# Optimization experiments

Measured on AMD Instinct MI355X. Metric: run time of the kernel, lower is better.

Reference implementation:

```python
import jax, jax.numpy as jnp
import numpy as np

B, S, D, DIM = 8, 4096, 1024, 512  # batch, src nodes, dst nodes, feature dim


def setup_inputs() -> dict:
    key = jax.random.key(0)
    k1, k2, k3, k4, k5 = jax.random.split(key, 5)
    scale = 1.0 / np.sqrt(DIM)
    return {
        "src_val": jax.random.normal(k1, (B, S, DIM), dtype=jnp.float32),
        "src_state": jax.random.normal(k2, (B, S), dtype=jnp.float32),
        "dst_val": jax.random.normal(k3, (B, D, DIM), dtype=jnp.float32),
        "W_route": jax.random.normal(k4, (DIM, DIM), dtype=jnp.float32) * scale,
        "W_val": jax.random.normal(k5, (DIM, DIM), dtype=jnp.float32) * scale,
    }


def reference(src_val, src_state, dst_val, W_route, W_val):
    # Pairwise route logits: bilinear bipartite attention, [B, S, D]
    inv_sqrt_d = 1.0 / jnp.sqrt(jnp.asarray(src_val.shape[-1], src_val.dtype))
    q = jnp.einsum("bsd,de->bse", src_val, W_route)
    logits = jnp.einsum("bse,bke->bsk", q, dst_val) * inv_sqrt_d
    # route compression: softmax over dst nodes (dim=-1)
    routes = jax.nn.softmax(logits, axis=-1)
    # projections
    projected_val = jnp.einsum("bsd,de->bse", src_val, W_val)  # [B, S, DIM]
    projected_state = src_state                                 # identity state proj, [B, S]
    sender_strength = jax.nn.softplus(src_state)                # [B, S]
    # weighted routing + accumulation
    weighted_routes = routes * sender_strength[..., None]       # [B, S, D]
    delta_state = jnp.einsum("bsk,bs->bk", weighted_routes, projected_state)   # [B, D]
    delta_val = jnp.einsum("bsk,bsd->bkd", weighted_routes, projected_val)     # [B, D, DIM]
    return delta_state, delta_val
```

## Files before the change

### kernel.cpp

```cpp
#include <hip/hip_runtime.h>
#include <hip/hip_fp16.h>

#define B_   8
#define S_   4096
#define DD_  1024
#define DIM_ 512
#define SCALE 0.044194173824159216f

typedef __bf16 bf16x8 __attribute__((ext_vector_type(8)));
typedef float  floatx4 __attribute__((ext_vector_type(4)));

__device__ inline unsigned short f2bf(float f) {
    union { float f; unsigned int u; } v; v.f = f;
    unsigned int r = v.u + 0x7fffu + ((v.u >> 16) & 1u);
    return (unsigned short)(r >> 16);
}
__device__ inline float bf2f(unsigned short h) {
    union { unsigned int u; float f; } v; v.u = ((unsigned int)h) << 16;
    return v.f;
}
__device__ inline uint4 cvt8(const float* __restrict__ g) {
    float4 f0 = *(const float4*)g;
    float4 f1 = *(const float4*)(g + 4);
    unsigned short tmp[8] = {f2bf(f0.x), f2bf(f0.y), f2bf(f0.z), f2bf(f0.w),
                             f2bf(f1.x), f2bf(f1.y), f2bf(f1.z), f2bf(f1.w)};
    return *(const uint4*)tmp;
}
__device__ inline void async16(unsigned short* lds, const unsigned short* g) {
    __builtin_amdgcn_global_load_lds(
        (const __attribute__((address_space(1))) void*)g,
        (__attribute__((address_space(3))) void*)lds, 16, 0, 0);
}

__device__ inline void vwait8() { asm volatile("s_waitcnt vmcnt(8)" ::: "memory"); }
__device__ inline void vwait4() { asm volatile("s_waitcnt vmcnt(4)" ::: "memory"); }
__device__ inline void vwait0() { asm volatile("s_waitcnt vmcnt(0)" ::: "memory"); }
#define SBAR   __builtin_amdgcn_s_barrier()
#define SCHED0 __builtin_amdgcn_sched_barrier(0)

__device__ inline void mainloop256(unsigned short* As, unsigned short* Bs,
                                   const unsigned short* __restrict__ Ap, size_t lda,
                                   const unsigned short* __restrict__ Bp, size_t ldb,
                                   int nk, floatx4 (&acc)[8][4]) {
    const int t = threadIdx.x, lane = t & 63, w = t >> 6;
    const int wm = w >> 2, wn = w & 3;
    const int fr = lane & 15;
    const int swz  = (((lane >> 4) ^ ((fr >> 1) & 3)) << 3);
    const int csrc = (((t & 3) ^ ((t >> 3) & 3)) << 3);

    const unsigned short* gA = Ap + (size_t)(t >> 2) * lda + csrc;
    const unsigned short* gB = Bp + (size_t)(t >> 2) * ldb + csrc;
    unsigned short* ldsA = As + w * 512;
    unsigned short* ldsB = Bs + w * 512;

    auto stgA = [&](int buf, int kt, int kh) {
        const unsigned short* g = gA + (size_t)kt * 64 + kh * 32;
        async16(ldsA + buf * 16384 + kh * 8192,        g);
        async16(ldsA + buf * 16384 + kh * 8192 + 4096, g + (size_t)128 * lda);
    };
    auto stgB = [&](int buf, int kt, int kh) {
        const unsigned short* g = gB + (size_t)kt * 64 + kh * 32;
        async16(ldsB + buf * 16384 + kh * 8192,        g);
        async16(ldsB + buf * 16384 + kh * 8192 + 4096, g + (size_t)128 * ldb);
    };

    stgA(0, 0, 0); stgB(0, 0, 0); stgA(0, 0, 1); stgB(0, 0, 1);
    stgA(1, 1, 0); stgB(1, 1, 0);
    vwait8();
    SCHED0;
    SBAR;

    const int arow = wm * 128 + fr, brow = wn * 64 + fr;
    for (int kt = 0; kt < nk; ++kt) {
        const int cur = kt & 1;
        const bool sA = kt + 1 < nk, sB = kt + 2 < nk;
        const int base = cur * 16384;
        bf16x8 a[4], b[4], a2[4];
#pragma unroll
        for (int i = 0; i < 4; ++i)
            a[i] = *(const bf16x8*)&As[base + (arow + i * 16) * 32 + swz];
#pragma unroll
        for (int j = 0; j < 4; ++j)
            b[j] = *(const bf16x8*)&Bs[base + (brow + j * 16) * 32 + swz];
        if (sA) stgA(cur ^ 1, kt + 1, 1);
        SCHED0;
        SBAR;
        __builtin_amdgcn_s_setprio(1);
#pragma unroll
        for (int i = 0; i < 4; ++i)
#pragma unroll
            for (int j = 0; j < 4; ++j)
                acc[i][j] = __builtin_amdgcn_mfma_f32_16x16x32_bf16(a[i], b[j], acc[i][j], 0, 0, 0);
        __builtin_amdgcn_s_setprio(0);
        SBAR;
#pragma unroll
        for (int i = 0; i < 4; ++i)
            a2[i] = *(const bf16x8*)&As[base + (arow + 64 + i * 16) * 32 + swz];
        if (sA) stgB(cur ^ 1, kt + 1, 1);
        SCHED0;
        SBAR;
        __builtin_amdgcn_s_setprio(1);
#pragma unroll
        for (int i = 0; i < 4; ++i)
#pragma unroll
            for (int j = 0; j < 4; ++j)
                acc[4 + i][j] = __builtin_amdgcn_mfma_f32_16x16x32_bf16(a2[i], b[j], acc[4 + i][j], 0, 0, 0);
        __builtin_amdgcn_s_setprio(0);
        if (sA) vwait8(); else vwait0();
        SBAR;
#pragma unroll
        for (int i = 0; i < 4; ++i)
            a[i] = *(const bf16x8*)&As[base + 8192 + (arow + i * 16) * 32 + swz];
#pragma unroll
        for (int j = 0; j < 4; ++j)
            b[j] = *(const bf16x8*)&Bs[base + 8192 + (brow + j * 16) * 32 + swz];
        if (sB) stgA(cur, kt + 2, 0);
        SCHED0;
        SBAR;
        __builtin_amdgcn_s_setprio(1);
#pragma unroll
        for (int i = 0; i < 4; ++i)
#pragma unroll
            for (int j = 0; j < 4; ++j)
                acc[i][j] = __builtin_amdgcn_mfma_f32_16x16x32_bf16(a[i], b[j], acc[i][j], 0, 0, 0);
        __builtin_amdgcn_s_setprio(0);
        SBAR;
#pragma unroll
        for (int i = 0; i < 4; ++i)
            a2[i] = *(const bf16x8*)&As[base + 8192 + (arow + 64 + i * 16) * 32 + swz];
        if (sB) stgB(cur, kt + 2, 0);
        SCHED0;
        SBAR;
        __builtin_amdgcn_s_setprio(1);
#pragma unroll
        for (int i = 0; i < 4; ++i)
#pragma unroll
            for (int j = 0; j < 4; ++j)
                acc[4 + i][j] = __builtin_amdgcn_mfma_f32_16x16x32_bf16(a2[i], b[j], acc[4 + i][j], 0, 0, 0);
        __builtin_amdgcn_s_setprio(0);
        if (sA) { if (sB) vwait8(); else vwait4(); }
        SBAR;
    }
}

#define ACC_INIT8                                           \
    floatx4 acc[8][4];                                      \
    _Pragma("unroll") for (int i = 0; i < 8; ++i)           \
        _Pragma("unroll") for (int j = 0; j < 4; ++j)       \
            acc[i][j] = (floatx4){0.f, 0.f, 0.f, 0.f};

template <int AF32, int BF32>
__device__ inline void mainloop(unsigned short* As, unsigned short* Bs,
                                const void* Ap, size_t lda,
                                const void* Bp, size_t ldb,
                                int kIters, floatx4 (&acc)[4][4]) {
    const int t = threadIdx.x, lane = t & 63, wave = t >> 6;
    const int rA = t >> 2;
    const int cA = ((t & 3) ^ ((t >> 3) & 3)) * 8;
    const int mrow = (wave >> 1) * 64, ncol = (wave & 1) * 64;
    const int fr = lane & 15, fk = (lane >> 4) * 8;
    const int swz = (((fk >> 3) ^ ((fr >> 1) & 3)) << 3);

    const unsigned short* gA16 = nullptr; const float* gA32 = nullptr;
    const unsigned short* gB16 = nullptr; const float* gB32 = nullptr;
    if (AF32) gA32 = (const float*)Ap + (size_t)rA * lda + cA;
    else      gA16 = (const unsigned short*)Ap + (size_t)rA * lda + cA;
    if (BF32) gB32 = (const float*)Bp + (size_t)rA * ldb + cA;
    else      gB16 = (const unsigned short*)Bp + (size_t)rA * ldb + cA;

    unsigned short* ldsA = As + wave * 512;
    unsigned short* ldsB = Bs + wave * 512;

    auto stage = [&](int buf) {
        const int o = buf * 4096;
        if (AF32) {
            *(uint4*)&As[o + t * 8]        = cvt8(gA32);
            *(uint4*)&As[o + 2048 + t * 8] = cvt8(gA32 + 64 * lda);
            gA32 += 32;
        } else {
            async16(ldsA + o,        gA16);
            async16(ldsA + o + 2048, gA16 + 64 * lda);
            gA16 += 32;
        }
        if (BF32) {
            *(uint4*)&Bs[o + t * 8]        = cvt8(gB32);
            *(uint4*)&Bs[o + 2048 + t * 8] = cvt8(gB32 + 64 * ldb);
            gB32 += 32;
        } else {
            async16(ldsB + o,        gB16);
            async16(ldsB + o + 2048, gB16 + 64 * ldb);
            gB16 += 32;
        }
    };

    stage(0);
    __syncthreads();
    for (int kt = 0; kt < kIters; ++kt) {
        if (kt + 1 < kIters) stage((kt + 1) & 1);
        const int cur = (kt & 1) * 4096;
        bf16x8 af[4], bfr[4];
#pragma unroll
        for (int i = 0; i < 4; ++i)
            af[i] = *(const bf16x8*)&As[cur + (mrow + i * 16 + fr) * 32 + swz];
#pragma unroll
        for (int j = 0; j < 4; ++j)
            bfr[j] = *(const bf16x8*)&Bs[cur + (ncol + j * 16 + fr) * 32 + swz];
#pragma unroll
        for (int i = 0; i < 4; ++i)
#pragma unroll
            for (int j = 0; j < 4; ++j)
                acc[i][j] = __builtin_amdgcn_mfma_f32_16x16x32_bf16(af[i], bfr[j],
                                                                    acc[i][j], 0, 0, 0);
        __syncthreads();
    }
}

#define EPILOGUE_COORDS                                     \
    const int lane = threadIdx.x & 63, wave = threadIdx.x >> 6; \
    const int mrow = (wave >> 1) * 64, ncol = (wave & 1) * 64;  \
    const int col = lane & 15, q = lane >> 4;

#define ACC_INIT                                            \
    floatx4 acc[4][4];                                      \
    _Pragma("unroll") for (int i = 0; i < 4; ++i)           \
        _Pragma("unroll") for (int j = 0; j < 4; ++j)       \
            acc[i][j] = (floatx4){0.f, 0.f, 0.f, 0.f};

__global__ __launch_bounds__(256) void k_prep(const float* __restrict__ src,
                                              unsigned short* __restrict__ srcb) {
    const size_t idx = ((size_t)blockIdx.x * 256 + threadIdx.x) * 8;
    *(uint4*)&srcb[idx] = cvt8(src + idx);
}

__global__ __launch_bounds__(256) void k_dstWr(const float* __restrict__ dst,
                                               const float* __restrict__ Wr,
                                               unsigned short* __restrict__ DW) {
    __shared__ unsigned short As[2 * 128 * 32];
    __shared__ unsigned short Bs[2 * 128 * 32];
    const int n0 = blockIdx.x * 128, m0 = blockIdx.y * 128;
    ACC_INIT
    mainloop<1, 1>(As, Bs, dst + (size_t)m0 * DIM_, DIM_,
                   Wr + (size_t)n0 * DIM_, DIM_, DIM_ / 32, acc);
    EPILOGUE_COORDS
#pragma unroll
    for (int i = 0; i < 4; ++i)
#pragma unroll
        for (int j = 0; j < 4; ++j)
#pragma unroll
            for (int r = 0; r < 4; ++r)
                DW[(size_t)(m0 + mrow + i * 16 + q * 4 + r) * DIM_ +
                   n0 + ncol + j * 16 + col] = f2bf(acc[i][j][r] * SCALE);
}

__global__ __launch_bounds__(512) void k_logitsT(const unsigned short* __restrict__ DW,
                                                 const unsigned short* __restrict__ srcb,
                                                 unsigned short* __restrict__ LTb,
                                                 float* __restrict__ Lpart) {
    __shared__ __align__(16) unsigned short As[32768];
    __shared__ __align__(16) unsigned short Bs[32768];
    const int n = blockIdx.x;
    const int b = n & 7;
    const int rem = n >> 3;
    const int xs = rem >> 2;
    const int yd = rem & 3;
    const int n0 = xs * 256, m0 = yd * 256;
    ACC_INIT8
    mainloop256(As, Bs,
                DW + (size_t)b * DD_ * DIM_ + (size_t)m0 * DIM_, DIM_,
                srcb + (size_t)b * S_ * DIM_ + (size_t)n0 * DIM_, DIM_,
                DIM_ / 64, acc);
    const int t = threadIdx.x, lane = t & 63, w = t >> 6;
    const int wm = w >> 2, wn = w & 3;
    const int c16 = lane & 15, q = lane >> 4;
    const int row0 = m0 + wm * 128, col0 = n0 + wn * 64;
    unsigned short* LT = LTb + (size_t)b * DD_ * S_;
    float psum[4] = {0.f, 0.f, 0.f, 0.f};
#pragma unroll
    for (int i = 0; i < 8; ++i)
#pragma unroll
        for (int j = 0; j < 4; ++j)
#pragma unroll
            for (int r = 0; r < 4; ++r) {
                float e = __expf(acc[i][j][r]);
                LT[(size_t)(row0 + i * 16 + q * 4 + r) * S_ +
                   col0 + j * 16 + c16] = f2bf(e);
                psum[j] += e;
            }
    float* csum = (float*)As;
    const int slice = wm * 4 + q;
#pragma unroll
    for (int j = 0; j < 4; ++j)
        csum[slice * 256 + wn * 64 + j * 16 + c16] = psum[j];
    __syncthreads();
    if (t < 256) {
        float v = 0.f;
#pragma unroll
        for (int k = 0; k < 8; ++k) v += csum[k * 256 + t];
        Lpart[((size_t)b * 4 + yd) * S_ + n0 + t] = v;
    }
}

__global__ __launch_bounds__(256) void k_finalize(const float* __restrict__ state,
                                                  const float* __restrict__ Lpart,
                                                  float* __restrict__ scale) {
    const int i = blockIdx.x * 256 + threadIdx.x;
    const int b = i >> 12, s = i & (S_ - 1);
    float d = 0.f;
#pragma unroll
    for (int k = 0; k < 4; ++k) d += Lpart[((size_t)b * 4 + k) * S_ + s];
    const float st = state[i];
    const float sp = (st > 15.f) ? st : log1pf(__expf(st));
    scale[i] = sp / d;
}

__global__ __launch_bounds__(256) void k_srcT(const unsigned short* __restrict__ srcb,
                                              const float* __restrict__ scale,
                                              unsigned short* __restrict__ srcST) {
    __shared__ unsigned short Ts[64 * 65];
    const int s0 = blockIdx.x * 64, d0 = blockIdx.y * 64, b = blockIdx.z;
    const int t = threadIdx.x;
    {
        const int r = t >> 2, c0 = (t & 3) * 16;
        const unsigned short* g =
            srcb + (size_t)b * S_ * DIM_ + (size_t)(s0 + r) * DIM_ + d0 + c0;
        uint4 v0 = *(const uint4*)g;
        uint4 v1 = *(const uint4*)(g + 8);
        const unsigned short* e0 = (const unsigned short*)&v0;
        const unsigned short* e1 = (const unsigned short*)&v1;
        const float sc = scale[(size_t)b * S_ + s0 + r];
#pragma unroll
        for (int i = 0; i < 8; ++i) {
            Ts[r * 65 + c0 + i]     = f2bf(bf2f(e0[i]) * sc);
            Ts[r * 65 + c0 + 8 + i] = f2bf(bf2f(e1[i]) * sc);
        }
    }
    __syncthreads();
    {
        const int rr = t >> 2, c0 = (t & 3) * 16;
        unsigned short tmp[16];
#pragma unroll
        for (int j = 0; j < 16; ++j) tmp[j] = Ts[(c0 + j) * 65 + rr];
        unsigned short* o =
            srcST + (size_t)b * DIM_ * S_ + (size_t)(d0 + rr) * S_ + s0 + c0;
        *(uint4*)o = *(const uint4*)tmp;
        *(uint4*)(o + 8) = *(const uint4*)(tmp + 8);
    }
}

__global__ __launch_bounds__(256) void k_dstate(const unsigned short* __restrict__ LT,
                                                const float* __restrict__ state,
                                                const float* __restrict__ scale,
                                                float* __restrict__ out) {
    const int b = blockIdx.y;
    const int dd = blockIdx.x * 4 + (threadIdx.x >> 6);
    const int lane = threadIdx.x & 63;
    const unsigned short* row = LT + (size_t)b * DD_ * S_ + (size_t)dd * S_;
    const float* st = state + (size_t)b * S_;
    const float* sc = scale + (size_t)b * S_;

    float acc = 0.f;
#pragma unroll
    for (int it = 0; it < S_ / 512; ++it) {
        const int s = it * 512 + lane * 8;
        uint4 v = *(const uint4*)(row + s);
        const unsigned short* e = (const unsigned short*)&v;
        float4 f0 = *(const float4*)(st + s);
        float4 f1 = *(const float4*)(st + s + 4);
        float4 c0 = *(const float4*)(sc + s);
        float4 c1 = *(const float4*)(sc + s + 4);
        acc += bf2f(e[0]) * f0.x * c0.x + bf2f(e[1]) * f0.y * c0.y +
               bf2f(e[2]) * f0.z * c0.z + bf2f(e[3]) * f0.w * c0.w +
               bf2f(e[4]) * f1.x * c1.x + bf2f(e[5]) * f1.y * c1.y +
               bf2f(e[6]) * f1.z * c1.z + bf2f(e[7]) * f1.w * c1.w;
    }
#pragma unroll
    for (int off = 32; off; off >>= 1) acc += __shfl_down(acc, off);
    if (lane == 0) out[(size_t)b * DD_ + dd] = acc;
}

__global__ __launch_bounds__(512) void k_dU(const unsigned short* __restrict__ LTb,
                                            const unsigned short* __restrict__ srcST,
                                            __half* __restrict__ Pp) {
    __shared__ __align__(16) unsigned short As[32768];
    __shared__ __align__(16) unsigned short Bs[32768];
    const int n = blockIdx.x;
    const int qn = n >> 3;
    const int tile = qn & 7, zhi = qn >> 3;
    const int z = (n & 7) + 8 * zhi;
    const int b = z >> 2, ks = z & 3;
    const int xe = tile >> 2;
    const int yd = tile & 3;
    const int n0 = xe * 256, m0 = yd * 256;
    ACC_INIT8
    mainloop256(As, Bs,
                LTb + (size_t)b * DD_ * S_ + (size_t)m0 * S_ + ks * 1024, S_,
                srcST + (size_t)b * DIM_ * S_ + (size_t)n0 * S_ + ks * 1024, S_,
                1024 / 64, acc);
    const int t = threadIdx.x, lane = t & 63, w = t >> 6;
    const int wm = w >> 2, wn = w & 3;
    const int c16 = lane & 15, q = lane >> 4;
    const int row0 = m0 + wm * 128, col0 = n0 + wn * 64;
    __half* O = Pp + (size_t)ks * B_ * DD_ * DIM_ + (size_t)b * DD_ * DIM_;
#pragma unroll
    for (int i = 0; i < 8; ++i)
#pragma unroll
        for (int j = 0; j < 4; ++j)
#pragma unroll
            for (int r = 0; r < 4; ++r)
                O[(size_t)(row0 + i * 16 + q * 4 + r) * DIM_ +
                  col0 + j * 16 + c16] = __float2half(acc[i][j][r]);
}

__global__ __launch_bounds__(256) void k_reduceU(const __half* __restrict__ Pp,
                                                 unsigned short* __restrict__ U,
                                                 const float* __restrict__ Wv,
                                                 unsigned short* __restrict__ WvT) {
    __shared__ float Ts[64 * 68];
    const int t = threadIdx.x;
    if (blockIdx.x < 2048) {
        const size_t idx = ((size_t)blockIdx.x * 256 + t) * 8;
        const size_t n = (size_t)B_ * DD_ * DIM_;
        float o[8] = {0.f, 0.f, 0.f, 0.f, 0.f, 0.f, 0.f, 0.f};
#pragma unroll
        for (int ks = 0; ks < 4; ++ks) {
            uint4 v = *(const uint4*)(Pp + (size_t)ks * n + idx);
            const __half* h = (const __half*)&v;
#pragma unroll
            for (int j = 0; j < 8; ++j) o[j] += __half2float(h[j]);
        }
        unsigned short tmp[8];
#pragma unroll
        for (int j = 0; j < 8; ++j) tmp[j] = f2bf(o[j]);
        *(uint4*)&U[idx] = *(const uint4*)tmp;
        return;
    }
    const int n2 = blockIdx.x - 2048;
    const int d0 = (n2 & 7) * 64, e0 = (n2 >> 3) * 64;
    {
        const int r = t >> 2, c0 = (t & 3) * 16;
        const float* g = Wv + (size_t)(d0 + r) * DIM_ + e0 + c0;
#pragma unroll
        for (int i = 0; i < 4; ++i)
            *(float4*)&Ts[r * 68 + c0 + i * 4] = *(const float4*)(g + i * 4);
    }
    __syncthreads();
    {
        const int rr = t >> 2, c0 = (t & 3) * 16;
        unsigned short tmp[16];
#pragma unroll
        for (int j = 0; j < 16; ++j) tmp[j] = f2bf(Ts[(c0 + j) * 68 + rr]);
        unsigned short* o = WvT + (size_t)(e0 + rr) * DIM_ + d0 + c0;
        *(uint4*)o = *(const uint4*)tmp;
        *(uint4*)(o + 8) = *(const uint4*)(tmp + 8);
    }
}

__global__ __launch_bounds__(256) void k_dvalW(const unsigned short* __restrict__ U,
                                               const unsigned short* __restrict__ WvT,
                                               float* __restrict__ d_val) {
    __shared__ unsigned short As[2 * 128 * 32];
    __shared__ unsigned short Bs[2 * 128 * 32];
    const int n0 = blockIdx.x * 128, m0 = blockIdx.y * 128;
    ACC_INIT
    mainloop<0, 0>(As, Bs, U + (size_t)m0 * DIM_, DIM_,
                   WvT + (size_t)n0 * DIM_, DIM_, DIM_ / 32, acc);
    EPILOGUE_COORDS
#pragma unroll
    for (int i = 0; i < 4; ++i)
#pragma unroll
        for (int j = 0; j < 4; ++j)
#pragma unroll
            for (int r = 0; r < 4; ++r)
                d_val[(size_t)(m0 + mrow + i * 16 + q * 4 + r) * DIM_ +
                      n0 + ncol + j * 16 + col] = acc[i][j][r];
}

extern "C" void kernel_launch(void* const* d_in, const int* in_sizes, int n_in,
                              void* d_out, int out_size, void* d_ws, size_t ws_size,
                              hipStream_t stream) {
    const float* src   = (const float*)d_in[0];
    const float* state = (const float*)d_in[1];
    const float* dst   = (const float*)d_in[2];
    const float* Wr    = (const float*)d_in[3];
    const float* Wv    = (const float*)d_in[4];

    unsigned short* srcb = (unsigned short*)d_ws;
    __half* Pp = (__half*)d_ws;
    unsigned short* LT = srcb + (size_t)B_ * S_ * DIM_;
    unsigned short* U  = LT;
    unsigned short* WvT = U + (size_t)B_ * DD_ * DIM_;
    unsigned short* C = LT + (size_t)B_ * DD_ * S_;
    unsigned short* DW = C;
    float* Lpart = (float*)(DW + (size_t)B_ * DD_ * DIM_);
    unsigned short* srcST = C;

    float* d_state = (float*)d_out;
    float* d_val   = (float*)d_out + B_ * DD_;
    float* scale   = d_val;

    k_prep<<<dim3(8192), 256, 0, stream>>>(src, srcb);
    k_dstWr<<<dim3(DIM_ / 128, (B_ * DD_) / 128), 256, 0, stream>>>(dst, Wr, DW);
    k_logitsT<<<dim3(512), 512, 0, stream>>>(DW, srcb, LT, Lpart);
    k_finalize<<<dim3((B_ * S_) / 256), 256, 0, stream>>>(state, Lpart, scale);
    k_dstate<<<dim3(DD_ / 4, B_), 256, 0, stream>>>(LT, state, scale, d_state);
    k_srcT<<<dim3(S_ / 64, DIM_ / 64, B_), 256, 0, stream>>>(srcb, scale, srcST);
    k_dU<<<dim3(256), 512, 0, stream>>>(LT, srcST, Pp);
    k_reduceU<<<dim3(2048 + 64), 256, 0, stream>>>(Pp, U, Wv, WvT);
    k_dvalW<<<dim3(DIM_ / 128, (B_ * DD_) / 128), 256, 0, stream>>>(U, WvT, d_val);
}
```

Measured before the change: 278.9 us.

## Software-pipeline LDS fragment loads with MFMA in 256-tile GEMM mainloop

Restructures the 256x256 GEMM main loop so each quarter-step's LDS fragment reads are issued alongside the previous quarter's MFMAs, with fragments for the next k-tile prefetched at the end of each iteration. This cuts the barriers per iteration from eight to four and relaxes the vmcnt waits from 8 to 6. Launch bounds on the two big GEMM kernels now request 2 blocks per CU. Holding more fragment registers live together with the occupancy hint risks register spills or tighter scheduling constraints.

```diff
diff --git a/kernel.cpp b/kernel.cpp
--- a/kernel.cpp
+++ b/kernel.cpp
@@ -32,9 +32,12 @@
         (__attribute__((address_space(3))) void*)lds, 16, 0, 0);
 }
 
-__device__ inline void vwait8() { asm volatile("s_waitcnt vmcnt(8)" ::: "memory"); }
-__device__ inline void vwait4() { asm volatile("s_waitcnt vmcnt(4)" ::: "memory"); }
-__device__ inline void vwait0() { asm volatile("s_waitcnt vmcnt(0)" ::: "memory"); }
+template <int N> __device__ inline void vwait() {
+    if constexpr (N == 0)      asm volatile("s_waitcnt vmcnt(0)" ::: "memory");
+    else if constexpr (N == 4) asm volatile("s_waitcnt vmcnt(4)" ::: "memory");
+    else if constexpr (N == 6) asm volatile("s_waitcnt vmcnt(6)" ::: "memory");
+    else                       asm volatile("s_waitcnt vmcnt(8)" ::: "memory");
+}
 #define SBAR   __builtin_amdgcn_s_barrier()
 #define SCHED0 __builtin_amdgcn_sched_barrier(0)
 
@@ -66,79 +69,82 @@
 
     stgA(0, 0, 0); stgB(0, 0, 0); stgA(0, 0, 1); stgB(0, 0, 1);
     stgA(1, 1, 0); stgB(1, 1, 0);
-    vwait8();
+    vwait<8>();
     SCHED0;
     SBAR;
 
     const int arow = wm * 128 + fr, brow = wn * 64 + fr;
+    bf16x8 a0[4], b0[4], a1[4], a2[4], b2[4], a3[4];
+#pragma unroll
+    for (int i = 0; i < 4; ++i) a0[i] = *(const bf16x8*)&As[(arow + i * 16) * 32 + swz];
+#pragma unroll
+    for (int j = 0; j < 4; ++j) b0[j] = *(const bf16x8*)&Bs[(brow + j * 16) * 32 + swz];
+
     for (int kt = 0; kt < nk; ++kt) {
-        const int cur = kt & 1;
+        const int cur = kt & 1, base = cur * 16384;
         const bool sA = kt + 1 < nk, sB = kt + 2 < nk;
-        const int base = cur * 16384;
-        bf16x8 a[4], b[4], a2[4];
-#pragma unroll
-        for (int i = 0; i < 4; ++i)
-            a[i] = *(const bf16x8*)&As[base + (arow + i * 16) * 32 + swz];
-#pragma unroll
-        for (int j = 0; j < 4; ++j)
-            b[j] = *(const bf16x8*)&Bs[base + (brow + j * 16) * 32 + swz];
         if (sA) stgA(cur ^ 1, kt + 1, 1);
         SCHED0;
+        __builtin_amdgcn_s_setprio(1);
+#pragma unroll
+        for (int i = 0; i < 4; ++i)
+            a1[i] = *(const bf16x8*)&As[base + (arow + 64 + i * 16) * 32 + swz];
+#pragma unroll
+        for (int i = 0; i < 4; ++i)
+#pragma unroll
+            for (int j = 0; j < 4; ++j)
+                acc[i][j] = __builtin_amdgcn_mfma_f32_16x16x32_bf16(a0[i], b0[j], acc[i][j], 0, 0, 0);
+        __builtin_amdgcn_s_setprio(0);
+        if (sA) vwait<6>(); else vwait<0>();
         SBAR;
+        if (sA) stgB(cur ^ 1, kt + 1, 1);
+        SCHED0;
         __builtin_amdgcn_s_setprio(1);
 #pragma unroll
         for (int i = 0; i < 4; ++i)
+            a2[i] = *(const bf16x8*)&As[base + 8192 + (arow + i * 16) * 32 + swz];
+#pragma unroll
+        for (int j = 0; j < 4; ++j)
+            b2[j] = *(const bf16x8*)&Bs[base + 8192 + (brow + j * 16) * 32 + swz];
+#pragma unroll
+        for (int i = 0; i < 4; ++i)
 #pragma unroll
             for (int j = 0; j < 4; ++j)
-                acc[i][j] = __builtin_amdgcn_mfma_f32_16x16x32_bf16(a[i], b[j], acc[i][j], 0, 0, 0);
+                acc[4 + i][j] = __builtin_amdgcn_mfma_f32_16x16x32_bf16(a1[i], b0[j], acc[4 + i][j], 0, 0, 0);
         __builtin_amdgcn_s_setprio(0);
         SBAR;
-#pragma unroll
-        for (int i = 0; i < 4; ++i)
-            a2[i] = *(const bf16x8*)&As[base + (arow + 64 + i * 16) * 32 + swz];
-        if (sA) stgB(cur ^ 1, kt + 1, 1);
-        SCHED0;
-        SBAR;
-        __builtin_amdgcn_s_setprio(1);
-#pragma unroll
-        for (int i = 0; i < 4; ++i)
-#pragma unroll
-            for (int j = 0; j < 4; ++j)
-                acc[4 + i][j] = __builtin_amdgcn_mfma_f32_16x16x32_bf16(a2[i], b[j], acc[4 + i][j], 0, 0, 0);
-        __builtin_amdgcn_s_setprio(0);
-        if (sA) vwait8(); else vwait0();
-        SBAR;
-#pragma unroll
-        for (int i = 0; i < 4; ++i)
-            a[i] = *(const bf16x8*)&As[base + 8192 + (arow + i * 16) * 32 + swz];
-#pragma unroll
-        for (int j = 0; j < 4; ++j)
-            b[j] = *(const bf16x8*)&Bs[base + 8192 + (brow + j * 16) * 32 + swz];
         if (sB) stgA(cur, kt + 2, 0);
         SCHED0;
+        __builtin_amdgcn_s_setprio(1);
+#pragma unroll
+        for (int i = 0; i < 4; ++i)
+            a3[i] = *(const bf16x8*)&As[base + 8192 + (arow + 64 + i * 16) * 32 + swz];
+#pragma unroll
+        for (int i = 0; i < 4; ++i)
+#pragma unroll
+            for (int j = 0; j < 4; ++j)
+                acc[i][j] = __builtin_amdgcn_mfma_f32_16x16x32_bf16(a2[i], b2[j], acc[i][j], 0, 0, 0);
+        __builtin_amdgcn_s_setprio(0);
+        if (sA) { if (sB) vwait<6>(); else vwait<4>(); }
         SBAR;
-        __builtin_amdgcn_s_setprio(1);
-#pragma unroll
-        for (int i = 0; i < 4; ++i)
-#pragma unroll
-            for (int j = 0; j < 4; ++j)
-                acc[i][j] = __builtin_amdgcn_mfma_f32_16x16x32_bf16(a[i], b[j], acc[i][j], 0, 0, 0);
-        __builtin_amdgcn_s_setprio(0);
-        SBAR;
-#pragma unroll
-        for (int i = 0; i < 4; ++i)
-            a2[i] = *(const bf16x8*)&As[base + 8192 + (arow + 64 + i * 16) * 32 + swz];
         if (sB) stgB(cur, kt + 2, 0);
         SCHED0;
-        SBAR;
         __builtin_amdgcn_s_setprio(1);
-#pragma unroll
-        for (int i = 0; i < 4; ++i)
+        if (sA) {
+            const int nb = (cur ^ 1) * 16384;
+#pragma unroll
+            for (int i = 0; i < 4; ++i)
+                a0[i] = *(const bf16x8*)&As[nb + (arow + i * 16) * 32 + swz];
 #pragma unroll
             for (int j = 0; j < 4; ++j)
-                acc[4 + i][j] = __builtin_amdgcn_mfma_f32_16x16x32_bf16(a2[i], b[j], acc[4 + i][j], 0, 0, 0);
+                b0[j] = *(const bf16x8*)&Bs[nb + (brow + j * 16) * 32 + swz];
+        }
+#pragma unroll
+        for (int i = 0; i < 4; ++i)
+#pragma unroll
+            for (int j = 0; j < 4; ++j)
+                acc[4 + i][j] = __builtin_amdgcn_mfma_f32_16x16x32_bf16(a3[i], b2[j], acc[4 + i][j], 0, 0, 0);
         __builtin_amdgcn_s_setprio(0);
-        if (sA) { if (sB) vwait8(); else vwait4(); }
         SBAR;
     }
 }
@@ -252,10 +258,10 @@
                    n0 + ncol + j * 16 + col] = f2bf(acc[i][j][r] * SCALE);
 }
 
-__global__ __launch_bounds__(512) void k_logitsT(const unsigned short* __restrict__ DW,
-                                                 const unsigned short* __restrict__ srcb,
-                                                 unsigned short* __restrict__ LTb,
-                                                 float* __restrict__ Lpart) {
+__global__ __launch_bounds__(512, 2) void k_logitsT(const unsigned short* __restrict__ DW,
+                                                    const unsigned short* __restrict__ srcb,
+                                                    unsigned short* __restrict__ LTb,
+                                                    float* __restrict__ Lpart) {
     __shared__ __align__(16) unsigned short As[32768];
     __shared__ __align__(16) unsigned short Bs[32768];
     const int n = blockIdx.x;
@@ -378,9 +384,9 @@
     if (lane == 0) out[(size_t)b * DD_ + dd] = acc;
 }
 
-__global__ __launch_bounds__(512) void k_dU(const unsigned short* __restrict__ LTb,
-                                            const unsigned short* __restrict__ srcST,
-                                            __half* __restrict__ Pp) {
+__global__ __launch_bounds__(512, 2) void k_dU(const unsigned short* __restrict__ LTb,
+                                               const unsigned short* __restrict__ srcST,
+                                               __half* __restrict__ Pp) {
     __shared__ __align__(16) unsigned short As[32768];
     __shared__ __align__(16) unsigned short Bs[32768];
     const int n = blockIdx.x;
```

Result: faster. 272.3 us (-2.4%).
